# Performance work log

Measured on AMD Instinct MI355X. Metric: run time of the kernel, lower is better.

The kernel has to match this reference:

```python
import jax, jax.numpy as jnp
import numpy as np
from jax import lax

B, C, H, W = 32, 4, 84, 84
A, N, D = 8, 20000, 128
P = 50          # kNN neighbors used by each DND
DELTA = 1e-3    # inverse-distance kernel delta


def _conv(x, w, stride):
    return lax.conv_general_dilated(
        x, w, window_strides=(stride, stride), padding='VALID',
        dimension_numbers=('NCHW', 'OIHW', 'NCHW'))


def embed(states, conv1_w, conv1_b, conv2_w, conv2_b, conv3_w, conv3_b, fc_w, fc_b):
    x = jax.nn.relu(_conv(states, conv1_w, 4) + conv1_b[None, :, None, None])  # [B,32,20,20]
    x = jax.nn.relu(_conv(x, conv2_w, 2) + conv2_b[None, :, None, None])       # [B,64,9,9]
    x = jax.nn.relu(_conv(x, conv3_w, 1) + conv3_b[None, :, None, None])       # [B,64,7,7]
    x = x.reshape(x.shape[0], -1)                                              # [B,3136]
    return x @ fc_w.T + fc_b                                                   # [B,128] keys


def setup_inputs() -> dict:
    key = jax.random.key(0)
    ks = jax.random.split(key, 9)
    sc = lambda fan_in: 1.0 / np.sqrt(fan_in)
    return {
        'states': jax.random.normal(ks[0], (B, C, H, W), jnp.float32),
        'actions': jax.random.randint(ks[1], (B,), 0, A, jnp.int64 if jax.config.jax_enable_x64 else jnp.int32),
        'conv1_w': jax.random.normal(ks[2], (32, 4, 8, 8), jnp.float32) * sc(4 * 64),
        'conv1_b': jnp.zeros((32,), jnp.float32),
        'conv2_w': jax.random.normal(ks[3], (64, 32, 4, 4), jnp.float32) * sc(32 * 16),
        'conv2_b': jnp.zeros((64,), jnp.float32),
        'conv3_w': jax.random.normal(ks[4], (64, 64, 3, 3), jnp.float32) * sc(64 * 9),
        'conv3_b': jnp.zeros((64,), jnp.float32),
        'fc_w': jax.random.normal(ks[5], (D, 3136), jnp.float32) * sc(3136),
        'fc_b': jnp.zeros((D,), jnp.float32),
        'dnd_keys': jax.random.normal(ks[6], (A, N, D), jnp.float32),
        'dnd_values': jax.random.normal(ks[7], (A, N), jnp.float32),
    }


def reference(states, actions, conv1_w, conv1_b, conv2_w, conv2_b, conv3_w, conv3_b,
              fc_w, fc_b, dnd_keys, dnd_values):
    h = embed(states, conv1_w, conv1_b, conv2_w, conv2_b, conv3_w, conv3_b, fc_w, fc_b)  # [B,D]
    # Route each sample to its action's DND memory (batched gather).
    tab_k = dnd_keys[actions]    # [B,N,D]
    tab_v = dnd_values[actions]  # [B,N]
    # Squared L2 distances via expansion (avoids [B,N,D] diff intermediate).
    d2 = (jnp.sum(h * h, -1)[:, None]
          - 2.0 * jnp.einsum('bd,bnd->bn', h, tab_k)
          + jnp.sum(tab_k * tab_k, -1))  # [B,N]
    neg_top, idx = lax.top_k(-d2, P)     # P nearest neighbors per sample
    top_d2 = jnp.maximum(-neg_top, 0.0)
    w = 1.0 / (top_d2 + DELTA)           # inverse-distance kernel
    w = w / jnp.sum(w, -1, keepdims=True)
    v = jnp.take_along_axis(tab_v, idx, axis=1)  # [B,P]
    q = jnp.sum(w * v, -1)               # [B]
    return q
```

## Files before the change

kernel.cpp:

```cpp
#include <hip/hip_runtime.h>

#define BB 32
#define AA 8
#define NN 20000
#define DD 128
#define PP 50
#define DELTA 1e-3f

typedef unsigned long long ull;

__global__ __launch_bounds__(256) void conv1_k(const float* __restrict__ x,
                                               const float* __restrict__ w,
                                               const float* __restrict__ bias,
                                               float* __restrict__ y) {
    int idx = blockIdx.x * 256 + threadIdx.x;
    if (idx >= 32 * 32 * 20 * 20) return;
    int ox = idx % 20;
    int t = idx / 20;
    int oy = t % 20; t /= 20;
    int oc = t % 32;
    int b = t / 32;
    float acc = bias[oc];
    const float* xb = x + (size_t)b * 4 * 84 * 84;
    const float* wk = w + oc * 4 * 64;
    for (int ic = 0; ic < 4; ic++) {
        const float* xc = xb + ic * 84 * 84 + (oy * 4) * 84 + ox * 4;
        const float* wc = wk + ic * 64;
#pragma unroll
        for (int ky = 0; ky < 8; ky++) {
            const float4* xr = (const float4*)(xc + ky * 84);
            const float4* wr = (const float4*)(wc + ky * 8);
            float4 x0 = xr[0], x1 = xr[1];
            float4 w0 = wr[0], w1 = wr[1];
            acc += x0.x * w0.x + x0.y * w0.y + x0.z * w0.z + x0.w * w0.w
                 + x1.x * w1.x + x1.y * w1.y + x1.z * w1.z + x1.w * w1.w;
        }
    }
    y[idx] = fmaxf(acc, 0.f);
}

__global__ __launch_bounds__(256) void conv2_k(const float* __restrict__ x,
                                               const float* __restrict__ w,
                                               const float* __restrict__ bias,
                                               float* __restrict__ y) {
    int idx = blockIdx.x * 256 + threadIdx.x;
    if (idx >= 32 * 64 * 9 * 9) return;
    int ox = idx % 9;
    int t = idx / 9;
    int oy = t % 9; t /= 9;
    int oc = t % 64;
    int b = t / 64;
    float acc = bias[oc];
    const float* xb = x + (size_t)b * 32 * 400;
    const float* wk = w + oc * 32 * 16;
    for (int ic = 0; ic < 32; ic++) {
        const float* xc = xb + ic * 400 + (oy * 2) * 20 + ox * 2;
        const float* wc = wk + ic * 16;
#pragma unroll
        for (int ky = 0; ky < 4; ky++) {
            const float2* xr = (const float2*)(xc + ky * 20);
            float2 x0 = xr[0], x1 = xr[1];
            float4 wv = ((const float4*)(wc + ky * 4))[0];
            acc += x0.x * wv.x + x0.y * wv.y + x1.x * wv.z + x1.y * wv.w;
        }
    }
    y[idx] = fmaxf(acc, 0.f);
}

__global__ __launch_bounds__(256) void conv3_k(const float* __restrict__ x,
                                               const float* __restrict__ w,
                                               const float* __restrict__ bias,
                                               float* __restrict__ y) {
    int idx = blockIdx.x * 256 + threadIdx.x;
    if (idx >= 32 * 64 * 7 * 7) return;
    int ox = idx % 7;
    int t = idx / 7;
    int oy = t % 7; t /= 7;
    int oc = t % 64;
    int b = t / 64;
    float acc = bias[oc];
    const float* xb = x + (size_t)b * 64 * 81;
    const float* wk = w + oc * 64 * 9;
    for (int ic = 0; ic < 64; ic++) {
        const float* xc = xb + ic * 81 + oy * 9 + ox;
        const float* wc = wk + ic * 9;
#pragma unroll
        for (int ky = 0; ky < 3; ky++)
#pragma unroll
            for (int kx = 0; kx < 3; kx++)
                acc += xc[ky * 9 + kx] * wc[ky * 3 + kx];
    }
    y[idx] = fmaxf(acc, 0.f);
}

__global__ __launch_bounds__(256) void fc_k(const float* __restrict__ x,
                                            const float* __restrict__ w,
                                            const float* __restrict__ bias,
                                            float* __restrict__ h) {
    __shared__ float sx[3136];
    int b = blockIdx.x >> 3;
    int g = blockIdx.x & 7;
    int tid = threadIdx.x;
    const float4* xr = (const float4*)(x + (size_t)b * 3136);
    float4* sx4w = (float4*)sx;
    for (int i = tid; i < 784; i += 256) sx4w[i] = xr[i];
    __syncthreads();
    int oc_local = tid >> 4;
    int kslice = tid & 15;
    int oc = g * 16 + oc_local;
    const float4* wr = (const float4*)(w + (size_t)oc * 3136);
    const float4* sx4 = (const float4*)sx;
    float acc = 0.f;
#pragma unroll 7
    for (int j = 0; j < 49; j++) {
        int i = kslice + 16 * j;
        float4 a = sx4[i], c = wr[i];
        acc += a.x * c.x + a.y * c.y + a.z * c.z + a.w * c.w;
    }
#pragma unroll
    for (int m = 8; m >= 1; m >>= 1) acc += __shfl_xor(acc, m);
    if (kslice == 0) h[b * 128 + oc] = acc + bias[oc];
}

__global__ __launch_bounds__(256) void dist2_k(const float* __restrict__ h,
                                               const int* __restrict__ actions,
                                               const float* __restrict__ keys,
                                               float* __restrict__ d2) {
    int b = blockIdx.y;
    int a = actions[b];
    int tid = threadIdx.x;
    int hw = tid >> 5;
    int l32 = tid & 31;
    float4 hv = ((const float4*)(h + b * DD))[l32];
    const float* kb = keys + (size_t)a * NN * DD;
    int r0 = blockIdx.x * 40 + hw * 5;
    float s0, s1, s2, s3, s4;
    {
        float4 k0 = ((const float4*)(kb + (size_t)(r0 + 0) * DD))[l32];
        float4 k1 = ((const float4*)(kb + (size_t)(r0 + 1) * DD))[l32];
        float4 k2 = ((const float4*)(kb + (size_t)(r0 + 2) * DD))[l32];
        float4 k3 = ((const float4*)(kb + (size_t)(r0 + 3) * DD))[l32];
        float4 k4 = ((const float4*)(kb + (size_t)(r0 + 4) * DD))[l32];
        float dx, dy, dz, dw;
        dx = hv.x - k0.x; dy = hv.y - k0.y; dz = hv.z - k0.z; dw = hv.w - k0.w;
        s0 = dx * dx + dy * dy + dz * dz + dw * dw;
        dx = hv.x - k1.x; dy = hv.y - k1.y; dz = hv.z - k1.z; dw = hv.w - k1.w;
        s1 = dx * dx + dy * dy + dz * dz + dw * dw;
        dx = hv.x - k2.x; dy = hv.y - k2.y; dz = hv.z - k2.z; dw = hv.w - k2.w;
        s2 = dx * dx + dy * dy + dz * dz + dw * dw;
        dx = hv.x - k3.x; dy = hv.y - k3.y; dz = hv.z - k3.z; dw = hv.w - k3.w;
        s3 = dx * dx + dy * dy + dz * dz + dw * dw;
        dx = hv.x - k4.x; dy = hv.y - k4.y; dz = hv.z - k4.z; dw = hv.w - k4.w;
        s4 = dx * dx + dy * dy + dz * dz + dw * dw;
    }
#pragma unroll
    for (int m = 16; m >= 1; m >>= 1) {
        s0 += __shfl_xor(s0, m);
        s1 += __shfl_xor(s1, m);
        s2 += __shfl_xor(s2, m);
        s3 += __shfl_xor(s3, m);
        s4 += __shfl_xor(s4, m);
    }
    if (l32 == 0) {
        float* dst = d2 + (size_t)b * NN + r0;
        dst[0] = s0; dst[1] = s1; dst[2] = s2; dst[3] = s3; dst[4] = s4;
    }
}

__global__ __launch_bounds__(1024) void select_k(const float* __restrict__ d2,
                                                 const float* __restrict__ values,
                                                 const int* __restrict__ actions,
                                                 float* __restrict__ q) {
    const int NB = 8160;
    const int CAP = 512;
    int b = blockIdx.x, tid = threadIdx.x;
    int lane = tid & 63, wave = tid >> 6;
    __shared__ int hist[NB];
    __shared__ int fhist[1024];
    __shared__ float cd[CAP];
    __shared__ int ci[CAP];
    __shared__ int scounter;
    __shared__ int s_t, s_below;
    __shared__ int s_ft;
    __shared__ int wsum[16];
    __shared__ float rw[16], rwv[16];

    const float* db = d2 + (size_t)b * NN;
    for (int i = tid; i < NB; i += 1024) hist[i] = 0;
    fhist[tid] = 0;
    if (tid == 0) scounter = 0;
    __syncthreads();

    for (int i = tid; i < NN; i += 1024)
        atomicAdd(&hist[__float_as_uint(db[i]) >> 18], 1);
    __syncthreads();

    {
        int s = 0;
#pragma unroll
        for (int u = 0; u < 8; u++) s += hist[tid * 8 + u];
        int sc = s;
#pragma unroll
        for (int m = 1; m < 64; m <<= 1) {
            int o = __shfl_up(sc, m);
            if (lane >= m) sc += o;
        }
        if (lane == 63) wsum[wave] = sc;
        __syncthreads();
        if (tid < 16) {
            int vc = wsum[tid];
            for (int m = 1; m < 16; m <<= 1) {
                int o = __shfl_up(vc, m);
                if (tid >= m) vc += o;
            }
            wsum[tid] = vc;
        }
        __syncthreads();
        int incl = ((wave == 0) ? 0 : wsum[wave - 1]) + sc;
        int excl = incl - s;
        if (excl < PP && incl >= PP) {
            int c = excl;
#pragma unroll
            for (int u = 0; u < 8; u++) {
                int bkt = tid * 8 + u;
                int hv = hist[bkt];
                if (c < PP && c + hv >= PP) { s_t = bkt; s_below = c; }
                c += hv;
            }
        }
    }
    __syncthreads();
    int t = s_t, below = s_below;

    for (int i = tid; i < NN; i += 1024) {
        unsigned bits = __float_as_uint(db[i]);
        if ((int)(bits >> 18) == t) atomicAdd(&fhist[(bits >> 8) & 1023], 1);
    }
    __syncthreads();

    {
        int s = fhist[tid];
        int sc = s;
#pragma unroll
        for (int m = 1; m < 64; m <<= 1) {
            int o = __shfl_up(sc, m);
            if (lane >= m) sc += o;
        }
        if (lane == 63) wsum[wave] = sc;
        __syncthreads();
        if (tid < 16) {
            int vc = wsum[tid];
            for (int m = 1; m < 16; m <<= 1) {
                int o = __shfl_up(vc, m);
                if (tid >= m) vc += o;
            }
            wsum[tid] = vc;
        }
        __syncthreads();
        int incl = ((wave == 0) ? 0 : wsum[wave - 1]) + sc;
        int excl = incl - s;
        if (below + excl < PP && below + incl >= PP) s_ft = tid;
    }
    __syncthreads();
    int ft = s_ft;

    for (int i = tid; i < NN; i += 1024) {
        unsigned bits = __float_as_uint(db[i]);
        int c = (int)(bits >> 18);
        bool take = (c < t) || (c == t && (int)((bits >> 8) & 1023) <= ft);
        if (take) {
            int slot = atomicAdd(&scounter, 1);
            if (slot < CAP) { cd[slot] = db[i]; ci[slot] = i; }
        }
    }
    __syncthreads();
    int k = min(scounter, CAP);

    float w = 0.f, wv = 0.f;
    int a = actions[b];
    for (int s = tid; s < k; s += 1024) {
        ull key = ((ull)__float_as_uint(cd[s]) << 32) | (unsigned)ci[s];
        int cnt = 0;
        for (int j = 0; j < k; j++) {
            ull kj = ((ull)__float_as_uint(cd[j]) << 32) | (unsigned)ci[j];
            cnt += (kj < key);
        }
        if (cnt < PP) {
            float dd = fmaxf(cd[s], 0.f);
            float ww = 1.f / (dd + DELTA);
            w += ww;
            wv += ww * values[(size_t)a * NN + ci[s]];
        }
    }
#pragma unroll
    for (int m = 32; m >= 1; m >>= 1) {
        w += __shfl_xor(w, m);
        wv += __shfl_xor(wv, m);
    }
    if (lane == 0) { rw[wave] = w; rwv[wave] = wv; }
    __syncthreads();
    if (tid < 16) {
        float tw = rw[tid], twv = rwv[tid];
#pragma unroll
        for (int m = 8; m >= 1; m >>= 1) {
            tw += __shfl_xor(tw, m);
            twv += __shfl_xor(twv, m);
        }
        if (tid == 0) q[b] = twv / tw;
    }
}

extern "C" void kernel_launch(void* const* d_in, const int* in_sizes, int n_in,
                              void* d_out, int out_size, void* d_ws, size_t ws_size,
                              hipStream_t stream) {
    const float* states = (const float*)d_in[0];
    const int* actions = (const int*)d_in[1];
    const float* c1w = (const float*)d_in[2];
    const float* c1b = (const float*)d_in[3];
    const float* c2w = (const float*)d_in[4];
    const float* c2b = (const float*)d_in[5];
    const float* c3w = (const float*)d_in[6];
    const float* c3b = (const float*)d_in[7];
    const float* fcw = (const float*)d_in[8];
    const float* fcb = (const float*)d_in[9];
    const float* keys = (const float*)d_in[10];
    const float* vals = (const float*)d_in[11];
    float* out = (float*)d_out;

    float* ws = (float*)d_ws;
    float* c1o = ws;
    float* c2o = c1o + 409600;
    float* c3o = c2o + 165888;
    float* h   = c3o + 100352;
    float* d2  = h + 4096;

    conv1_k<<<(409600 + 255) / 256, 256, 0, stream>>>(states, c1w, c1b, c1o);
    conv2_k<<<(165888 + 255) / 256, 256, 0, stream>>>(c1o, c2w, c2b, c2o);
    conv3_k<<<(100352 + 255) / 256, 256, 0, stream>>>(c2o, c3w, c3b, c3o);
    fc_k<<<256, 256, 0, stream>>>(c3o, fcw, fcb, h);
    dist2_k<<<dim3(500, BB), 256, 0, stream>>>(h, actions, keys, d2);
    select_k<<<BB, 1024, 0, stream>>>(d2, vals, actions, out);
}
```

Baseline: 257.3 us.

## Group samples by action so each DND key tile is read once

Adds a routing kernel that buckets batch samples by action, then computes distances per action table. Each block loads a 160-row key tile once and reuses it for every sample routed to that action, with the sample embeddings staged in shared memory. This is meant to replace the per-sample re-reads of the key table (32 samples over 8 tables) with a single pass per table. In exchange it adds a launch, makes per-block work depend on how actions are distributed, and leaves blocks for unused actions idle.

```diff
diff --git a/kernel.cpp b/kernel.cpp
--- a/kernel.cpp
+++ b/kernel.cpp
@@ -122,48 +122,80 @@
     if (kslice == 0) h[b * 128 + oc] = acc + bias[oc];
 }
 
-__global__ __launch_bounds__(256) void dist2_k(const float* __restrict__ h,
-                                               const int* __restrict__ actions,
+__global__ __launch_bounds__(64) void route_k(const int* __restrict__ actions,
+                                              int* __restrict__ cnt,
+                                              int* __restrict__ list) {
+    int lane = threadIdx.x;
+    int act = (lane < BB) ? actions[lane] : -1;
+#pragma unroll
+    for (int a = 0; a < AA; a++) {
+        ull mask = __ballot(act == a);
+        if (act == a) {
+            int pos = __popcll(mask & ((1ull << lane) - 1));
+            list[a * BB + pos] = lane;
+        }
+        if (lane == a) cnt[a] = __popcll(mask);
+    }
+}
+
+__global__ __launch_bounds__(256) void dist3_k(const float* __restrict__ h,
+                                               const int* __restrict__ cnt,
+                                               const int* __restrict__ list,
                                                const float* __restrict__ keys,
                                                float* __restrict__ d2) {
-    int b = blockIdx.y;
-    int a = actions[b];
+    int a = blockIdx.y;
+    int m = cnt[a];
+    if (m == 0) return;
     int tid = threadIdx.x;
+    __shared__ float hl[BB * DD];
+    __shared__ int sl[BB];
+    if (tid < BB) sl[tid] = list[a * BB + tid];
+    __syncthreads();
+    for (int i = tid; i < m * DD; i += 256) {
+        int j = i >> 7;
+        hl[i] = h[sl[j] * DD + (i & 127)];
+    }
+    __syncthreads();
+
     int hw = tid >> 5;
     int l32 = tid & 31;
-    float4 hv = ((const float4*)(h + b * DD))[l32];
     const float* kb = keys + (size_t)a * NN * DD;
-    int r0 = blockIdx.x * 40 + hw * 5;
-    float s0, s1, s2, s3, s4;
-    {
-        float4 k0 = ((const float4*)(kb + (size_t)(r0 + 0) * DD))[l32];
-        float4 k1 = ((const float4*)(kb + (size_t)(r0 + 1) * DD))[l32];
-        float4 k2 = ((const float4*)(kb + (size_t)(r0 + 2) * DD))[l32];
-        float4 k3 = ((const float4*)(kb + (size_t)(r0 + 3) * DD))[l32];
-        float4 k4 = ((const float4*)(kb + (size_t)(r0 + 4) * DD))[l32];
-        float dx, dy, dz, dw;
-        dx = hv.x - k0.x; dy = hv.y - k0.y; dz = hv.z - k0.z; dw = hv.w - k0.w;
-        s0 = dx * dx + dy * dy + dz * dz + dw * dw;
-        dx = hv.x - k1.x; dy = hv.y - k1.y; dz = hv.z - k1.z; dw = hv.w - k1.w;
-        s1 = dx * dx + dy * dy + dz * dz + dw * dw;
-        dx = hv.x - k2.x; dy = hv.y - k2.y; dz = hv.z - k2.z; dw = hv.w - k2.w;
-        s2 = dx * dx + dy * dy + dz * dz + dw * dw;
-        dx = hv.x - k3.x; dy = hv.y - k3.y; dz = hv.z - k3.z; dw = hv.w - k3.w;
-        s3 = dx * dx + dy * dy + dz * dz + dw * dw;
-        dx = hv.x - k4.x; dy = hv.y - k4.y; dz = hv.z - k4.z; dw = hv.w - k4.w;
-        s4 = dx * dx + dy * dy + dz * dz + dw * dw;
-    }
-#pragma unroll
-    for (int m = 16; m >= 1; m >>= 1) {
-        s0 += __shfl_xor(s0, m);
-        s1 += __shfl_xor(s1, m);
-        s2 += __shfl_xor(s2, m);
-        s3 += __shfl_xor(s3, m);
-        s4 += __shfl_xor(s4, m);
-    }
-    if (l32 == 0) {
-        float* dst = d2 + (size_t)b * NN + r0;
-        dst[0] = s0; dst[1] = s1; dst[2] = s2; dst[3] = s3; dst[4] = s4;
+    const float4* hl4 = (const float4*)hl;
+    int r0 = blockIdx.x * 160 + hw * 20;
+
+    for (int rr = 0; rr < 20; rr += 5) {
+        int r = r0 + rr;
+        float4 k0 = ((const float4*)(kb + (size_t)(r + 0) * DD))[l32];
+        float4 k1 = ((const float4*)(kb + (size_t)(r + 1) * DD))[l32];
+        float4 k2 = ((const float4*)(kb + (size_t)(r + 2) * DD))[l32];
+        float4 k3 = ((const float4*)(kb + (size_t)(r + 3) * DD))[l32];
+        float4 k4 = ((const float4*)(kb + (size_t)(r + 4) * DD))[l32];
+        for (int j = 0; j < m; j++) {
+            float4 hv = hl4[j * 32 + l32];
+            float dx, dy, dz, dw, s0, s1, s2, s3, s4;
+            dx = hv.x - k0.x; dy = hv.y - k0.y; dz = hv.z - k0.z; dw = hv.w - k0.w;
+            s0 = dx * dx + dy * dy + dz * dz + dw * dw;
+            dx = hv.x - k1.x; dy = hv.y - k1.y; dz = hv.z - k1.z; dw = hv.w - k1.w;
+            s1 = dx * dx + dy * dy + dz * dz + dw * dw;
+            dx = hv.x - k2.x; dy = hv.y - k2.y; dz = hv.z - k2.z; dw = hv.w - k2.w;
+            s2 = dx * dx + dy * dy + dz * dz + dw * dw;
+            dx = hv.x - k3.x; dy = hv.y - k3.y; dz = hv.z - k3.z; dw = hv.w - k3.w;
+            s3 = dx * dx + dy * dy + dz * dz + dw * dw;
+            dx = hv.x - k4.x; dy = hv.y - k4.y; dz = hv.z - k4.z; dw = hv.w - k4.w;
+            s4 = dx * dx + dy * dy + dz * dz + dw * dw;
+#pragma unroll
+            for (int mm = 16; mm >= 1; mm >>= 1) {
+                s0 += __shfl_xor(s0, mm);
+                s1 += __shfl_xor(s1, mm);
+                s2 += __shfl_xor(s2, mm);
+                s3 += __shfl_xor(s3, mm);
+                s4 += __shfl_xor(s4, mm);
+            }
+            if (l32 == 0) {
+                float* dst = d2 + (size_t)sl[j] * NN + r;
+                dst[0] = s0; dst[1] = s1; dst[2] = s2; dst[3] = s3; dst[4] = s4;
+            }
+        }
     }
 }
 
@@ -333,11 +365,14 @@
     float* c3o = c2o + 165888;
     float* h   = c3o + 100352;
     float* d2  = h + 4096;
+    int* cnt   = (int*)(d2 + 640000);
+    int* list  = cnt + 8;
 
     conv1_k<<<(409600 + 255) / 256, 256, 0, stream>>>(states, c1w, c1b, c1o);
     conv2_k<<<(165888 + 255) / 256, 256, 0, stream>>>(c1o, c2w, c2b, c2o);
     conv3_k<<<(100352 + 255) / 256, 256, 0, stream>>>(c2o, c3w, c3b, c3o);
     fc_k<<<256, 256, 0, stream>>>(c3o, fcw, fcb, h);
-    dist2_k<<<dim3(500, BB), 256, 0, stream>>>(h, actions, keys, d2);
+    route_k<<<1, 64, 0, stream>>>(actions, cnt, list);
+    dist3_k<<<dim3(125, AA), 256, 0, stream>>>(h, cnt, list, keys, d2);
     select_k<<<BB, 1024, 0, stream>>>(d2, vals, actions, out);
 }
```

Measured after the change: 247.7 us. -3.7%, faster.

## Group samples by action and reuse LDS key tiles across all matching samples

Applied to the files above, without the earlier changes.

The distance kernel now launches one block per 64-row key tile per action, instead of one per sample. Each block finds the samples routed to its action, stages their embeddings and a swizzled tile of 64 key rows in shared memory, then computes distances for every matching sample from that tile. Each key row is read from global memory once per action rather than once per sample, which cuts the dominant key traffic. In exchange, per-thread compute becomes serial over 128 dims, and load balance depends on how many samples share each action.

```diff
diff --git a/kernel.cpp b/kernel.cpp
--- a/kernel.cpp
+++ b/kernel.cpp
@@ -122,48 +122,65 @@
     if (kslice == 0) h[b * 128 + oc] = acc + bias[oc];
 }
 
-__global__ __launch_bounds__(256) void dist2_k(const float* __restrict__ h,
+__global__ __launch_bounds__(256) void dist4_k(const float* __restrict__ h,
                                                const int* __restrict__ actions,
                                                const float* __restrict__ keys,
                                                float* __restrict__ d2) {
-    int b = blockIdx.y;
-    int a = actions[b];
+    int a = blockIdx.y;
     int tid = threadIdx.x;
-    int hw = tid >> 5;
-    int l32 = tid & 31;
-    float4 hv = ((const float4*)(h + b * DD))[l32];
-    const float* kb = keys + (size_t)a * NN * DD;
-    int r0 = blockIdx.x * 40 + hw * 5;
-    float s0, s1, s2, s3, s4;
-    {
-        float4 k0 = ((const float4*)(kb + (size_t)(r0 + 0) * DD))[l32];
-        float4 k1 = ((const float4*)(kb + (size_t)(r0 + 1) * DD))[l32];
-        float4 k2 = ((const float4*)(kb + (size_t)(r0 + 2) * DD))[l32];
-        float4 k3 = ((const float4*)(kb + (size_t)(r0 + 3) * DD))[l32];
-        float4 k4 = ((const float4*)(kb + (size_t)(r0 + 4) * DD))[l32];
-        float dx, dy, dz, dw;
-        dx = hv.x - k0.x; dy = hv.y - k0.y; dz = hv.z - k0.z; dw = hv.w - k0.w;
-        s0 = dx * dx + dy * dy + dz * dz + dw * dw;
-        dx = hv.x - k1.x; dy = hv.y - k1.y; dz = hv.z - k1.z; dw = hv.w - k1.w;
-        s1 = dx * dx + dy * dy + dz * dz + dw * dw;
-        dx = hv.x - k2.x; dy = hv.y - k2.y; dz = hv.z - k2.z; dw = hv.w - k2.w;
-        s2 = dx * dx + dy * dy + dz * dz + dw * dw;
-        dx = hv.x - k3.x; dy = hv.y - k3.y; dz = hv.z - k3.z; dw = hv.w - k3.w;
-        s3 = dx * dx + dy * dy + dz * dz + dw * dw;
-        dx = hv.x - k4.x; dy = hv.y - k4.y; dz = hv.z - k4.z; dw = hv.w - k4.w;
-        s4 = dx * dx + dy * dy + dz * dz + dw * dw;
-    }
-#pragma unroll
-    for (int m = 16; m >= 1; m >>= 1) {
-        s0 += __shfl_xor(s0, m);
-        s1 += __shfl_xor(s1, m);
-        s2 += __shfl_xor(s2, m);
-        s3 += __shfl_xor(s3, m);
-        s4 += __shfl_xor(s4, m);
-    }
-    if (l32 == 0) {
-        float* dst = d2 + (size_t)b * NN + r0;
-        dst[0] = s0; dst[1] = s1; dst[2] = s2; dst[3] = s3; dst[4] = s4;
+    int lane = tid & 63, wave = tid >> 6;
+    __shared__ float4 tile[64 * 32];
+    __shared__ float4 hl4[BB * 32];
+    __shared__ int sl[BB];
+    __shared__ int s_m;
+
+    if (wave == 0) {
+        int act = (lane < BB) ? actions[lane] : -1;
+        ull mask = __ballot(act == a);
+        if (act == a) {
+            int pos = __popcll(mask & ((1ull << lane) - 1));
+            sl[pos] = lane;
+        }
+        if (lane == 0) s_m = __popcll(mask);
+    }
+    __syncthreads();
+    int m = s_m;
+    if (m == 0) return;
+
+    for (int i = tid; i < m * 32; i += 256) {
+        int s = i >> 5, g = i & 31;
+        hl4[i] = ((const float4*)(h + sl[s] * DD))[g];
+    }
+
+    int r0 = blockIdx.x * 64;
+    int valid = min(64, NN - r0);
+    const float4* kb4 = (const float4*)(keys + (size_t)a * NN * DD);
+#pragma unroll
+    for (int i = 0; i < 8; i++) {
+        int idx = i * 256 + tid;
+        int row = idx >> 5, g = idx & 31;
+        if (row < valid)
+            tile[row * 32 + ((g + (row & 31)) & 31)] = kb4[(size_t)(r0 + row) * 32 + g];
+    }
+    __syncthreads();
+
+    int row = lane;
+    if (row < valid) {
+        int c = row & 31;
+        const float4* trow = &tile[row * 32];
+        for (int s = wave; s < m; s += 4) {
+            const float4* hp = &hl4[s * 32];
+            float acc = 0.f;
+#pragma unroll 8
+            for (int g = 0; g < 32; g++) {
+                float4 kv = trow[(g + c) & 31];
+                float4 hv = hp[g];
+                float dx = hv.x - kv.x, dy = hv.y - kv.y;
+                float dz = hv.z - kv.z, dw = hv.w - kv.w;
+                acc += dx * dx + dy * dy + dz * dz + dw * dw;
+            }
+            d2[(size_t)sl[s] * NN + r0 + row] = acc;
+        }
     }
 }
 
@@ -338,6 +355,6 @@
     conv2_k<<<(165888 + 255) / 256, 256, 0, stream>>>(c1o, c2w, c2b, c2o);
     conv3_k<<<(100352 + 255) / 256, 256, 0, stream>>>(c2o, c3w, c3b, c3o);
     fc_k<<<256, 256, 0, stream>>>(c3o, fcw, fcb, h);
-    dist2_k<<<dim3(500, BB), 256, 0, stream>>>(h, actions, keys, d2);
+    dist4_k<<<dim3(313, AA), 256, 0, stream>>>(h, actions, keys, d2);
     select_k<<<BB, 1024, 0, stream>>>(d2, vals, actions, out);
 }
```

Measured after the change: 251.1 us. -2.4%, faster.
